# Kernel optimization log

Hardware: AMD Instinct MI355X
Metric: run time of the kernel (lower is better)

Reference implementation:

```python
import jax, jax.numpy as jnp
import numpy as np

BS, L, HIDDEN = 4, 2048, 1024
H, HD, R = 16, 64, 4


def setup_inputs() -> dict:
    key = jax.random.key(0)
    k1, k2, k3, k4 = jax.random.split(key, 4)
    hidden_states = jax.random.normal(k1, (BS, L, HIDDEN), dtype=jnp.float32)
    scale = np.float32(1.0 / np.sqrt(HIDDEN))
    Wk = jax.random.normal(k2, (HIDDEN, H * HD), dtype=jnp.float32) * scale
    bk = jnp.zeros((H * HD,), jnp.float32)
    Wv = jax.random.normal(k3, (HIDDEN, H * HD), dtype=jnp.float32) * scale
    bv = jnp.zeros((H * HD,), jnp.float32)
    xavier = np.float32(np.sqrt(2.0 / (H + HD)))  # xavier_normal_ for (H, HD)
    ReadingHead = jax.random.normal(k4, (H, HD), dtype=jnp.float32) * xavier
    bidirection_weight = jnp.full((H, 2 * R), 1.0 / (2 * R), jnp.float32)
    return dict(hidden_states=hidden_states, Wk=Wk, bk=bk, Wv=Wv, bv=bv,
                ReadingHead=ReadingHead, bidirection_weight=bidirection_weight)


def _shift_step(carry, x):
    # carry: [bs, R, H] int32 registers; x = (valid [bs, H] bool, slot0 scalar int32)
    v, s = x
    bs, r, nh = carry.shape
    shifted = jnp.concatenate([jnp.broadcast_to(s, (bs, 1, nh)).astype(carry.dtype),
                               carry[:, :-1, :]], axis=1)
    new = jnp.where(v[:, None, :], shifted, carry)
    return new, new


def _forward_regs(valid):
    # valid: [bs, L, H] bool -> register index map [bs, L, R, H]
    bs, length, nh = valid.shape
    init = jnp.zeros((bs, R, nh), jnp.int32)  # position 0 registers are 0
    xs = (jnp.moveaxis(valid[:, 1:, :], 1, 0), jnp.arange(1, length, dtype=jnp.int32))
    _, ys = jax.lax.scan(_shift_step, init, xs)
    regs = jnp.concatenate([init[None], ys], axis=0)  # [L, bs, R, H]
    return jnp.moveaxis(regs, 0, 1)


def _backward_regs(valid):
    # valid: [bs, L, H] bool -> register index map [bs, L, R, H]
    bs, length, nh = valid.shape
    last = jnp.where(valid[:, length - 1, :], jnp.int32(length - 1), jnp.int32(0))
    init = jnp.zeros((bs, R, nh), jnp.int32).at[:, 0, :].set(last)  # position L-1
    # scan over positions 1..L-2 in reverse; slot0 at position l is l+1
    xs = (jnp.moveaxis(valid[:, 1:length - 1, :], 1, 0),
          jnp.arange(2, length, dtype=jnp.int32))
    _, ys = jax.lax.scan(_shift_step, init, xs, reverse=True)
    regs = jnp.concatenate([jnp.zeros((1, bs, R, nh), jnp.int32), ys, init[None]], axis=0)
    return jnp.moveaxis(regs, 0, 1)


def _gather_regs(V, regs):
    # V: [bs, L, H, hd]; regs: [bs, L, R, H] -> [bs, H, L, R, hd]
    bs, length, nh, hd = V.shape
    Vt = jnp.moveaxis(V, 2, 1)                       # [bs, H, L, hd]
    idx = jnp.moveaxis(regs, 3, 1).reshape(bs, nh, length * R)
    g = jnp.take_along_axis(Vt, idx[..., None], axis=2)  # [bs, H, L*R, hd]
    return g.reshape(bs, nh, length, R, hd)


def reference(hidden_states, Wk, bk, Wv, bv, ReadingHead, bidirection_weight):
    bs, length, _ = hidden_states.shape
    K1 = jax.nn.relu(hidden_states @ Wk + bk).reshape(bs, length, H, HD)
    V1 = jax.nn.relu(hidden_states @ Wv + bv).reshape(bs, length, H, HD)
    dot = jnp.einsum('blhd,hd->blh', K1, ReadingHead)
    valid = dot > 0.5  # attn_var == 'default' branch
    reg_f = _forward_regs(valid)
    reg_b = _backward_regs(valid)
    Vf = _gather_regs(V1, reg_f)  # [bs, H, L, R, hd]
    Vb = _gather_regs(V1, reg_b)
    out = (jnp.einsum('bhlrd,hr->blhd', Vf, bidirection_weight[:, :R])
           + jnp.einsum('bhlrd,hr->blhd', Vb, bidirection_weight[:, R:]))
    return out.reshape(bs, length, H * HD)
```

## Files before the change

### kernel.cpp

```cpp
#include <hip/hip_runtime.h>
#include <hip/hip_bf16.h>
#include <stdint.h>

#define BS   4
#define LSEQ 2048
#define HID  1024
#define NH   16
#define HD   64
#define M_TOT (BS * LSEQ)
#define NKV   (NH * HD)
#define NIT   24

typedef __attribute__((ext_vector_type(8))) short short8x;
typedef __attribute__((ext_vector_type(4))) float f32x4;

__device__ __forceinline__ float relu_f(float x) { return x > 0.0f ? x : 0.0f; }

__device__ __forceinline__ ushort bf16_rne(float f) {
    uint32_t x = __float_as_uint(f);
    return (ushort)((x + 0x7FFFu + ((x >> 16) & 1u)) >> 16);
}
__device__ __forceinline__ float bf16_to_f(ushort h) {
    return __uint_as_float((uint32_t)h << 16);
}

__device__ __forceinline__ void gload_lds16(const void* g, void* l) {
    typedef __attribute__((address_space(1))) const uint32_t GU;
    typedef __attribute__((address_space(3))) uint32_t LU;
    __builtin_amdgcn_global_load_lds((GU*)g, (LU*)l, 16, 0, 0);
}

__global__ __launch_bounds__(256) void prep(
    const float* __restrict__ A,
    const float* __restrict__ Wv, const float* __restrict__ Wk,
    ushort* __restrict__ Ahi, ushort* __restrict__ Alo,
    ushort* __restrict__ WvhiT, ushort* __restrict__ WvloT,
    ushort* __restrict__ WkhiT, ushort* __restrict__ WkloT)
{
    __shared__ float t[64][65];
    const int bid = blockIdx.x;
    const int tid = threadIdx.x;
    if (bid < 8192) {
        int i = bid * 256 + tid;
        float4 v = ((const float4*)A)[i];
        ushort4 h, l;
        h.x = bf16_rne(v.x); l.x = bf16_rne(v.x - bf16_to_f(h.x));
        h.y = bf16_rne(v.y); l.y = bf16_rne(v.y - bf16_to_f(h.y));
        h.z = bf16_rne(v.z); l.z = bf16_rne(v.z - bf16_to_f(h.z));
        h.w = bf16_rne(v.w); l.w = bf16_rne(v.w - bf16_to_f(h.w));
        ((ushort4*)Ahi)[i] = h;
        ((ushort4*)Alo)[i] = l;
    } else {
        int idx = bid - 8192;
        const float* W  = (idx < 256) ? Wv : Wk;
        ushort* hiT     = (idx < 256) ? WvhiT : WkhiT;
        ushort* loT     = (idx < 256) ? WvloT : WkloT;
        int tt = idx & 255;
        int k0 = (tt >> 4) * 64, n0 = (tt & 15) * 64;
#pragma unroll
        for (int it = 0; it < 4; ++it) {
            int r = it * 16 + (tid >> 4);
            int c = (tid & 15) * 4;
            float4 v = *(const float4*)&W[(size_t)(k0 + r) * NKV + n0 + c];
            t[r][c] = v.x; t[r][c + 1] = v.y; t[r][c + 2] = v.z; t[r][c + 3] = v.w;
        }
        __syncthreads();
        int n  = tid >> 2;
        int kc = (tid & 3) * 16;
        ushort hb[16], lb[16];
#pragma unroll
        for (int j = 0; j < 16; ++j) {
            float f = t[kc + j][n];
            ushort h = bf16_rne(f);
            hb[j] = h;
            lb[j] = bf16_rne(f - bf16_to_f(h));
        }
        size_t o = (size_t)(n0 + n) * 1024 + k0 + kc;
        *(uint4*)&hiT[o]     = *(uint4*)&hb[0];
        *(uint4*)&hiT[o + 8] = *(uint4*)&hb[8];
        *(uint4*)&loT[o]     = *(uint4*)&lb[0];
        *(uint4*)&loT[o + 8] = *(uint4*)&lb[8];
    }
}

__global__ __launch_bounds__(512, 2) void mfma_gemm(
    const ushort* __restrict__ Ahi, const ushort* __restrict__ Alo,
    const ushort* __restrict__ WvhiT, const ushort* __restrict__ WvloT,
    const ushort* __restrict__ WkhiT, const ushort* __restrict__ WkloT,
    const float* __restrict__ bv, const float* __restrict__ bk,
    const float* __restrict__ RH,
    float* __restrict__ V1, unsigned char* __restrict__ validB)
{
    __shared__ ushort LA[2][256 * 64];
    __shared__ ushort LB[2][256 * 64];

    const int tid  = threadIdx.x;
    const int lane = tid & 63;
    const int wv   = tid >> 6;
    const int wm   = wv >> 2;
    const int wn   = wv & 3;
    const int bm   = blockIdx.x;
    const bool kpath = (blockIdx.y >= 4);
    const int bnl  = kpath ? (blockIdx.y - 4) : blockIdx.y;

    const ushort* Whi  = kpath ? WkhiT : WvhiT;
    const ushort* Wlo  = kpath ? WkloT : WvloT;
    const float*  bias = kpath ? bk : bv;

    f32x4 acc[8][4];
    const f32x4 zz = {0.f, 0.f, 0.f, 0.f};
#pragma unroll
    for (int i = 0; i < 8; ++i)
#pragma unroll
        for (int j = 0; j < 4; ++j) acc[i][j] = zz;

    const int rc0 = ((0 + (lane >> 4)) ^ (lane & 7)) * 8;
    const int rc1 = ((4 + (lane >> 4)) ^ (lane & 7)) * 8;

    auto Asrc = [&](int kt, int half) -> const ushort* {
        const ushort* base = ((kt >> 4) == 1) ? Alo : Ahi;
        return base + (size_t)(bm * 256 + half * 128) * 1024 + ((kt & 15) << 6);
    };
    auto Bsrc = [&](int kt, int half) -> const ushort* {
        const ushort* base = ((kt >> 4) == 2) ? Wlo : Whi;
        return base + (size_t)(bnl * 256 + half * 128) * 1024 + ((kt & 15) << 6);
    };

#define STAGE_HALF(dst, src) do {                                              \
    _Pragma("unroll")                                                          \
    for (int it_ = 0; it_ < 2; ++it_) {                                        \
        int f_ = it_ * 512 + tid;                                              \
        int r_ = f_ >> 3, c_ = f_ & 7;                                         \
        gload_lds16((src) + (size_t)r_ * 1024 + ((c_ ^ (r_ & 7)) << 3),        \
                    (dst) + (size_t)(it_ * 512 + wv * 64) * 8);                \
    }                                                                          \
} while (0)

#define READ_A(buf, half) do {                                                 \
    _Pragma("unroll")                                                          \
    for (int mi_ = 0; mi_ < 4; ++mi_) {                                        \
        int row_ = wm * 128 + (half) * 64 + mi_ * 16 + (lane & 15);            \
        const ushort* b_ = &LA[buf][row_ * 64];                                \
        a_f[mi_][0] = *(const short8x*)(b_ + rc0);                             \
        a_f[mi_][1] = *(const short8x*)(b_ + rc1);                             \
    }                                                                          \
} while (0)

#define READ_B(buf, half) do {                                                 \
    _Pragma("unroll")                                                          \
    for (int nj_ = 0; nj_ < 2; ++nj_) {                                        \
        int ni_ = (half) * 2 + nj_;                                            \
        int row_ = wn * 64 + ni_ * 16 + (lane & 15);                           \
        const ushort* b_ = &LB[buf][row_ * 64];                                \
        b_f[ni_][0] = *(const short8x*)(b_ + rc0);                             \
        b_f[ni_][1] = *(const short8x*)(b_ + rc1);                             \
    }                                                                          \
} while (0)

#define MFMA_QUAD(mh, nh) do {                                                 \
    _Pragma("unroll")                                                          \
    for (int k2_ = 0; k2_ < 2; ++k2_)                                          \
        _Pragma("unroll")                                                      \
        for (int mi_ = 0; mi_ < 4; ++mi_)                                      \
            _Pragma("unroll")                                                  \
            for (int nj_ = 0; nj_ < 2; ++nj_) {                                \
                int ni_ = (nh) * 2 + nj_;                                      \
                acc[(mh) * 4 + mi_][ni_] =                                     \
                    __builtin_amdgcn_mfma_f32_16x16x32_bf16(                   \
                        a_f[mi_][k2_], b_f[ni_][k2_], acc[(mh) * 4 + mi_][ni_],\
                        0, 0, 0);                                              \
            }                                                                  \
} while (0)

#define PHASE_SYNC()                                                           \
    __builtin_amdgcn_s_barrier();                                              \
    asm volatile("s_waitcnt lgkmcnt(0)" ::: "memory");                         \
    __builtin_amdgcn_sched_barrier(0);                                         \
    __builtin_amdgcn_s_setprio(1)

#define PHASE_END()                                                            \
    __builtin_amdgcn_s_setprio(0);                                             \
    __builtin_amdgcn_s_barrier()

    short8x a_f[4][2], b_f[4][2];

    STAGE_HALF(&LA[0][0],    Asrc(0, 0));
    STAGE_HALF(&LA[0][8192], Asrc(0, 1));
    STAGE_HALF(&LB[0][0],    Bsrc(0, 0));
    STAGE_HALF(&LB[0][8192], Bsrc(0, 1));
    STAGE_HALF(&LA[1][0],    Asrc(1, 0));
    STAGE_HALF(&LA[1][8192], Asrc(1, 1));
    STAGE_HALF(&LB[1][0],    Bsrc(1, 0));
    STAGE_HALF(&LB[1][8192], Bsrc(1, 1));
    asm volatile("s_waitcnt vmcnt(8)" ::: "memory");
    __builtin_amdgcn_s_barrier();

#pragma unroll 1
    for (int i = 0; i < NIT; ++i) {
        const int kt0 = 2 * i;
        const int kt1 = 2 * i + 1;
        const bool st = (i < NIT - 1);

        READ_A(0, 0); READ_B(0, 0);
        PHASE_SYNC();
        MFMA_QUAD(0, 0);
        PHASE_END();

        READ_B(0, 1);
        PHASE_SYNC();
        MFMA_QUAD(0, 1);
        PHASE_END();

        READ_A(0, 1);
        if (st) {
            STAGE_HALF(&LB[0][0],    Bsrc(kt0 + 2, 0));
            STAGE_HALF(&LB[0][8192], Bsrc(kt0 + 2, 1));
        }
        PHASE_SYNC();
        MFMA_QUAD(1, 1);
        PHASE_END();

        if (st) {
            STAGE_HALF(&LA[0][0],    Asrc(kt0 + 2, 0));
            STAGE_HALF(&LA[0][8192], Asrc(kt0 + 2, 1));
        }
        PHASE_SYNC();
        MFMA_QUAD(1, 0);
        __builtin_amdgcn_s_setprio(0);
        if (st) asm volatile("s_waitcnt vmcnt(8)" ::: "memory");
        else    asm volatile("s_waitcnt vmcnt(0)" ::: "memory");
        __builtin_amdgcn_s_barrier();

        READ_A(1, 0); READ_B(1, 0);
        PHASE_SYNC();
        MFMA_QUAD(0, 0);
        PHASE_END();

        READ_B(1, 1);
        PHASE_SYNC();
        MFMA_QUAD(0, 1);
        PHASE_END();

        READ_A(1, 1);
        if (st) {
            STAGE_HALF(&LB[1][0],    Bsrc(kt1 + 2, 0));
            STAGE_HALF(&LB[1][8192], Bsrc(kt1 + 2, 1));
        }
        PHASE_SYNC();
        MFMA_QUAD(1, 1);
        PHASE_END();

        if (st) {
            STAGE_HALF(&LA[1][0],    Asrc(kt1 + 2, 1 - 1));
            STAGE_HALF(&LA[1][8192], Asrc(kt1 + 2, 1));
        }
        PHASE_SYNC();
        MFMA_QUAD(1, 0);
        __builtin_amdgcn_s_setprio(0);
        if (st) asm volatile("s_waitcnt vmcnt(8)" ::: "memory");
        __builtin_amdgcn_s_barrier();
    }

    if (!kpath) {
#pragma unroll
        for (int mi = 0; mi < 8; ++mi)
#pragma unroll
            for (int ni = 0; ni < 4; ++ni) {
                int row0 = bm * 256 + wm * 128 + mi * 16 + (lane >> 4) * 4;
                int col  = bnl * 256 + wn * 64 + ni * 16 + (lane & 15);
                float bc = bias[col];
#pragma unroll
                for (int r = 0; r < 4; ++r)
                    V1[(size_t)(row0 + r) * NKV + col] = relu_f(acc[mi][ni][r] + bc);
            }
    } else {
        const int head = bnl * 4 + wn;
        float rhw[4], bcs[4];
#pragma unroll
        for (int ni = 0; ni < 4; ++ni) {
            int ch = ni * 16 + (lane & 15);
            rhw[ni] = RH[head * HD + ch];
            bcs[ni] = bias[head * HD + ch];
        }
#pragma unroll
        for (int mi = 0; mi < 8; ++mi) {
            float s[4];
#pragma unroll
            for (int r = 0; r < 4; ++r) {
                float v = 0.f;
#pragma unroll
                for (int ni = 0; ni < 4; ++ni)
                    v += relu_f(acc[mi][ni][r] + bcs[ni]) * rhw[ni];
                s[r] = v;
            }
#pragma unroll
            for (int m = 1; m < 16; m <<= 1)
#pragma unroll
                for (int r = 0; r < 4; ++r)
                    s[r] += __shfl_xor(s[r], m);
            if ((lane & 15) == 0) {
#pragma unroll
                for (int r = 0; r < 4; ++r) {
                    int grow = bm * 256 + wm * 128 + mi * 16 + (lane >> 4) * 4 + r;
                    int bb = grow >> 11, ll = grow & 2047;
                    validB[((size_t)bb * NH + head) * LSEQ + ll] = (s[r] > 0.5f) ? 1 : 0;
                }
            }
        }
    }
#undef STAGE_HALF
#undef READ_A
#undef READ_B
#undef MFMA_QUAD
#undef PHASE_SYNC
#undef PHASE_END
}

__global__ __launch_bounds__(256) void scan_kernel(
    const unsigned char* __restrict__ validB,
    short* __restrict__ idxb)
{
    const int bh = blockIdx.x;
    const int b  = bh >> 4;
    const int h  = bh & 15;
    const unsigned char* v = validB + ((size_t)b * NH + h) * LSEQ;

    __shared__ uint64_t words[LSEQ / 64];

    const int tid  = threadIdx.x;
    const int lane = tid & 63;
    const int wv   = tid >> 6;

#pragma unroll
    for (int it = 0; it < LSEQ / 256; ++it) {
        int p = it * 256 + wv * 64 + lane;
        uint64_t m = __ballot(v[p] != 0);
        if (lane == 0) {
            if ((p >> 6) == 0) m &= ~1ull;
            words[p >> 6] = m;
        }
    }
    __syncthreads();

#pragma unroll
    for (int it = 0; it < LSEQ / 256; ++it) {
        int l = it * 256 + tid;
        ushort f[4] = {0, 0, 0, 0};
        ushort g[4] = {0, 0, 0, 0};
        if (l > 0) {
            {
                int wi = l >> 6, bi = l & 63;
                uint64_t m = words[wi] & ((bi == 63) ? ~0ull : ((2ull << bi) - 1));
                int cnt = 0;
                while (cnt < 4) {
                    if (m == 0) { if (wi == 0) break; m = words[--wi]; continue; }
                    int p = 63 - __clzll(m);
                    f[cnt++] = (ushort)(wi * 64 + p);
                    m &= ~(1ull << p);
                }
            }
            {
                int wi = l >> 6, bi = l & 63;
                uint64_t m = words[wi] & (~0ull << bi);
                int cnt = 0;
                while (cnt < 4) {
                    if (m == 0) { if (wi == (LSEQ / 64) - 1) break; m = words[++wi]; continue; }
                    int p = __ffsll((long long)m) - 1;
                    int pos = wi * 64 + p;
                    g[cnt++] = (ushort)((pos >= LSEQ - 1) ? (LSEQ - 1) : (pos + 1));
                    m &= m - 1;
                }
            }
        }
        uint4 pk;
        pk.x = (uint32_t)f[0] | ((uint32_t)f[1] << 16);
        pk.y = (uint32_t)f[2] | ((uint32_t)f[3] << 16);
        pk.z = (uint32_t)g[0] | ((uint32_t)g[1] << 16);
        pk.w = (uint32_t)g[2] | ((uint32_t)g[3] << 16);
        *(uint4*)(idxb + (((size_t)(b * LSEQ + l)) * NH + h) * 8) = pk;
    }
}

__global__ __launch_bounds__(256) void gather_kernel(
    const float* __restrict__ V1,
    const short* __restrict__ idxb,
    const float* __restrict__ bw,
    float* __restrict__ out)
{
    int wid  = (blockIdx.x * 256 + threadIdx.x) >> 6;
    int lane = threadIdx.x & 63;
    int gr   = wid >> 4;
    int h    = wid & 15;
    int b    = gr >> 11;

    const ushort4* ip = (const ushort4*)(idxb + ((size_t)gr * NH + h) * 8);
    ushort4 i0 = ip[0];
    ushort4 i1 = ip[1];

    const float* wp    = bw + h * 8;
    const float* vbase = V1 + (size_t)b * LSEQ * NKV + h * HD + lane;

    float acc = wp[0] * vbase[(size_t)i0.x * NKV] + wp[1] * vbase[(size_t)i0.y * NKV] +
                wp[2] * vbase[(size_t)i0.z * NKV] + wp[3] * vbase[(size_t)i0.w * NKV] +
                wp[4] * vbase[(size_t)i1.x * NKV] + wp[5] * vbase[(size_t)i1.y * NKV] +
                wp[6] * vbase[(size_t)i1.z * NKV] + wp[7] * vbase[(size_t)i1.w * NKV];

    out[(size_t)gr * NKV + h * HD + lane] = acc;
}

extern "C" void kernel_launch(void* const* d_in, const int* in_sizes, int n_in,
                              void* d_out, int out_size, void* d_ws, size_t ws_size,
                              hipStream_t stream)
{
    const float* hs = (const float*)d_in[0];
    const float* Wk = (const float*)d_in[1];
    const float* bk = (const float*)d_in[2];
    const float* Wv = (const float*)d_in[3];
    const float* bv = (const float*)d_in[4];
    const float* RH = (const float*)d_in[5];
    const float* bw = (const float*)d_in[6];
    float* out = (float*)d_out;

    char* ws = (char*)d_ws;
    size_t o = 0;
    float* V1      = (float*)(ws + o);  o += (size_t)M_TOT * NKV * 4;
    ushort* Ahi    = (ushort*)(ws + o); o += (size_t)M_TOT * HID * 2;
    ushort* Alo    = (ushort*)(ws + o); o += (size_t)M_TOT * HID * 2;
    ushort* WvhiT  = (ushort*)(ws + o); o += (size_t)HID * NKV * 2;
    ushort* WvloT  = (ushort*)(ws + o); o += (size_t)HID * NKV * 2;
    ushort* WkhiT  = (ushort*)(ws + o); o += (size_t)HID * NKV * 2;
    ushort* WkloT  = (ushort*)(ws + o); o += (size_t)HID * NKV * 2;
    unsigned char* validB = (unsigned char*)(ws + o); o += (size_t)BS * NH * LSEQ;
    short* idxb    = (short*)(ws + o);  o += (size_t)M_TOT * NH * 8 * 2;

    prep<<<8192 + 512, 256, 0, stream>>>(hs, Wv, Wk, Ahi, Alo,
                                         WvhiT, WvloT, WkhiT, WkloT);
    mfma_gemm<<<dim3(M_TOT / 256, 8), 512, 0, stream>>>(
        Ahi, Alo, WvhiT, WvloT, WkhiT, WkloT, bv, bk, RH, V1, validB);
    scan_kernel<<<BS * NH, 256, 0, stream>>>(validB, idxb);
    gather_kernel<<<(M_TOT * NH) / 4, 256, 0, stream>>>(V1, idxb, bw, out);
}
```

Measured before the change: 228.2 us.

## Reschedule GEMM main loop with double A fragments and spread-out LDS staging

The GEMM main loop now reads both halves of the A fragments into two separate register sets (a_f, a2_f) early in each k-tile. All B fragments are also loaded in the first two phases, so the later MFMA phases need no LDS reads. Global-to-LDS staging is split into one half-tile per phase. The B tile for the odd k-step is staged just in time in the same iteration rather than two steps ahead, and the vmcnt waits are loosened accordingly. The goal is to overlap LDS reads and global loads more evenly with MFMA work, at the cost of extra VGPRs and a shorter prefetch distance for B.

Measured after the change: 229.9 us. Within noise of the previous version (+0.7%).

```diff
diff --git a/kernel.cpp b/kernel.cpp
--- a/kernel.cpp
+++ b/kernel.cpp
@@ -136,20 +136,20 @@
     }                                                                          \
 } while (0)
 
-#define READ_A(buf, half) do {                                                 \
+#define READ_A(buf, dst, half) do {                                            \
     _Pragma("unroll")                                                          \
     for (int mi_ = 0; mi_ < 4; ++mi_) {                                        \
         int row_ = wm * 128 + (half) * 64 + mi_ * 16 + (lane & 15);            \
         const ushort* b_ = &LA[buf][row_ * 64];                                \
-        a_f[mi_][0] = *(const short8x*)(b_ + rc0);                             \
-        a_f[mi_][1] = *(const short8x*)(b_ + rc1);                             \
+        dst[mi_][0] = *(const short8x*)(b_ + rc0);                             \
+        dst[mi_][1] = *(const short8x*)(b_ + rc1);                             \
     }                                                                          \
 } while (0)
 
-#define READ_B(buf, half) do {                                                 \
+#define READ_B2(buf, ni0) do {                                                 \
     _Pragma("unroll")                                                          \
     for (int nj_ = 0; nj_ < 2; ++nj_) {                                        \
-        int ni_ = (half) * 2 + nj_;                                            \
+        int ni_ = (ni0) + nj_;                                                 \
         int row_ = wn * 64 + ni_ * 16 + (lane & 15);                           \
         const ushort* b_ = &LB[buf][row_ * 64];                                \
         b_f[ni_][0] = *(const short8x*)(b_ + rc0);                             \
@@ -157,7 +157,7 @@
     }                                                                          \
 } while (0)
 
-#define MFMA_QUAD(mh, nh) do {                                                 \
+#define MFMA_QUAD(areg, mh, nh) do {                                           \
     _Pragma("unroll")                                                          \
     for (int k2_ = 0; k2_ < 2; ++k2_)                                          \
         _Pragma("unroll")                                                      \
@@ -167,7 +167,7 @@
                 int ni_ = (nh) * 2 + nj_;                                      \
                 acc[(mh) * 4 + mi_][ni_] =                                     \
                     __builtin_amdgcn_mfma_f32_16x16x32_bf16(                   \
-                        a_f[mi_][k2_], b_f[ni_][k2_], acc[(mh) * 4 + mi_][ni_],\
+                        areg[mi_][k2_], b_f[ni_][k2_], acc[(mh) * 4 + mi_][ni_],\
                         0, 0, 0);                                              \
             }                                                                  \
 } while (0)
@@ -182,7 +182,7 @@
     __builtin_amdgcn_s_setprio(0);                                             \
     __builtin_amdgcn_s_barrier()
 
-    short8x a_f[4][2], b_f[4][2];
+    short8x a_f[4][2], a2_f[4][2], b_f[4][2];
 
     STAGE_HALF(&LA[0][0],    Asrc(0, 0));
     STAGE_HALF(&LA[0][8192], Asrc(0, 1));
@@ -201,63 +201,53 @@
         const int kt1 = 2 * i + 1;
         const bool st = (i < NIT - 1);
 
-        READ_A(0, 0); READ_B(0, 0);
-        PHASE_SYNC();
-        MFMA_QUAD(0, 0);
-        PHASE_END();
-
-        READ_B(0, 1);
-        PHASE_SYNC();
-        MFMA_QUAD(0, 1);
-        PHASE_END();
-
-        READ_A(0, 1);
-        if (st) {
-            STAGE_HALF(&LB[0][0],    Bsrc(kt0 + 2, 0));
-            STAGE_HALF(&LB[0][8192], Bsrc(kt0 + 2, 1));
-        }
-        PHASE_SYNC();
-        MFMA_QUAD(1, 1);
-        PHASE_END();
-
-        if (st) {
-            STAGE_HALF(&LA[0][0],    Asrc(kt0 + 2, 0));
-            STAGE_HALF(&LA[0][8192], Asrc(kt0 + 2, 1));
-        }
-        PHASE_SYNC();
-        MFMA_QUAD(1, 0);
+        READ_A(0, a_f, 0); READ_B2(0, 0);
+        if (i > 0) STAGE_HALF(&LB[1][0], Bsrc(kt1, 0));
+        PHASE_SYNC();
+        MFMA_QUAD(a_f, 0, 0);
+        PHASE_END();
+
+        READ_A(0, a2_f, 1); READ_B2(0, 2);
+        if (i > 0) STAGE_HALF(&LB[1][8192], Bsrc(kt1, 1));
+        PHASE_SYNC();
+        MFMA_QUAD(a_f, 0, 1);
+        PHASE_END();
+
+        if (st) STAGE_HALF(&LA[0][0], Asrc(kt0 + 2, 0));
+        PHASE_SYNC();
+        MFMA_QUAD(a2_f, 1, 1);
+        PHASE_END();
+
+        if (st) STAGE_HALF(&LA[0][8192], Asrc(kt0 + 2, 1));
+        PHASE_SYNC();
+        MFMA_QUAD(a2_f, 1, 0);
         __builtin_amdgcn_s_setprio(0);
-        if (st) asm volatile("s_waitcnt vmcnt(8)" ::: "memory");
+        if (st) asm volatile("s_waitcnt vmcnt(4)" ::: "memory");
         else    asm volatile("s_waitcnt vmcnt(0)" ::: "memory");
         __builtin_amdgcn_s_barrier();
 
-        READ_A(1, 0); READ_B(1, 0);
-        PHASE_SYNC();
-        MFMA_QUAD(0, 0);
-        PHASE_END();
-
-        READ_B(1, 1);
-        PHASE_SYNC();
-        MFMA_QUAD(0, 1);
-        PHASE_END();
-
-        READ_A(1, 1);
-        if (st) {
-            STAGE_HALF(&LB[1][0],    Bsrc(kt1 + 2, 0));
-            STAGE_HALF(&LB[1][8192], Bsrc(kt1 + 2, 1));
-        }
-        PHASE_SYNC();
-        MFMA_QUAD(1, 1);
-        PHASE_END();
-
-        if (st) {
-            STAGE_HALF(&LA[1][0],    Asrc(kt1 + 2, 1 - 1));
-            STAGE_HALF(&LA[1][8192], Asrc(kt1 + 2, 1));
-        }
-        PHASE_SYNC();
-        MFMA_QUAD(1, 0);
+        READ_A(1, a_f, 0); READ_B2(1, 0);
+        if (st) STAGE_HALF(&LB[0][0], Bsrc(kt0 + 2, 0));
+        PHASE_SYNC();
+        MFMA_QUAD(a_f, 0, 0);
+        PHASE_END();
+
+        READ_A(1, a2_f, 1); READ_B2(1, 2);
+        if (st) STAGE_HALF(&LB[0][8192], Bsrc(kt0 + 2, 1));
+        PHASE_SYNC();
+        MFMA_QUAD(a_f, 0, 1);
+        PHASE_END();
+
+        if (st) STAGE_HALF(&LA[1][0], Asrc(kt1 + 2, 0));
+        PHASE_SYNC();
+        MFMA_QUAD(a2_f, 1, 1);
+        PHASE_END();
+
+        if (st) STAGE_HALF(&LA[1][8192], Asrc(kt1 + 2, 1));
+        PHASE_SYNC();
+        MFMA_QUAD(a2_f, 1, 0);
         __builtin_amdgcn_s_setprio(0);
-        if (st) asm volatile("s_waitcnt vmcnt(8)" ::: "memory");
+        if (st) asm volatile("s_waitcnt vmcnt(4)" ::: "memory");
         __builtin_amdgcn_s_barrier();
     }
 
@@ -310,7 +300,7 @@
     }
 #undef STAGE_HALF
 #undef READ_A
-#undef READ_B
+#undef READ_B2
 #undef MFMA_QUAD
 #undef PHASE_SYNC
 #undef PHASE_END
```
